# Kernel tuning notes

Measured on AMD Instinct MI355X. Metric: run time of the kernel, lower is better.

The kernel has to match this reference:

```python
import jax, jax.numpy as jnp
import numpy as np

ENCODER_DIM, DECODER_DIM, ATTENTION_DIM = 2048, 512, 512
B, L = 128, 196


def setup_inputs() -> dict:
    key = jax.random.key(0)
    ks = jax.random.split(key, 8)
    s_u = 1.0 / np.sqrt(ENCODER_DIM)
    s_w = 1.0 / np.sqrt(DECODER_DIM)
    s_a = 1.0 / np.sqrt(ATTENTION_DIM)
    return {
        "features": jax.random.normal(ks[0], (B, L, ENCODER_DIM), jnp.float32),
        "hidden_state": jax.random.normal(ks[1], (B, DECODER_DIM), jnp.float32),
        "U_w": jax.random.uniform(ks[2], (ENCODER_DIM, ATTENTION_DIM), jnp.float32, -s_u, s_u),
        "U_b": jax.random.uniform(ks[3], (ATTENTION_DIM,), jnp.float32, -s_u, s_u),
        "W_w": jax.random.uniform(ks[4], (DECODER_DIM, ATTENTION_DIM), jnp.float32, -s_w, s_w),
        "W_b": jax.random.uniform(ks[5], (ATTENTION_DIM,), jnp.float32, -s_w, s_w),
        "A_w": jax.random.uniform(ks[6], (ATTENTION_DIM,), jnp.float32, -s_a, s_a),
        "A_b": jax.random.uniform(ks[7], (1,), jnp.float32, -s_a, s_a),
    }


def reference(features, hidden_state, U_w, U_b, W_w, W_b, A_w, A_b):
    # u_hs: [B, L, A], w_ah: [B, A]
    u_hs = jnp.einsum('ble,ea->bla', features, U_w) + U_b
    w_ah = hidden_state @ W_w + W_b
    combined = jnp.tanh(u_hs + w_ah[:, None, :])          # [B, L, A]
    scores = jnp.einsum('bla,a->bl', combined, A_w) + A_b[0]  # [B, L]
    alpha = jax.nn.softmax(scores, axis=1)                 # [B, L]
    context = jnp.einsum('bl,ble->be', alpha, features)    # [B, E]
    return alpha, context
```

## Files before the change

### kernel.cpp

```cpp
#include <hip/hip_runtime.h>
#include <hip/hip_bf16.h>

#define ENC 2048
#define ADIM 512
#define DEC 512
#define NBATCH 128
#define NL 196
#define MTOT (NBATCH * NL)

typedef __attribute__((ext_vector_type(8))) short short8;
typedef __attribute__((ext_vector_type(4))) float f32x4;

__device__ __forceinline__ unsigned short f2bf(float f) {
    __hip_bfloat16 h = __float2bfloat16(f);
    union { __hip_bfloat16 h; unsigned short u; } cv; cv.h = h; return cv.u;
}
__device__ __forceinline__ unsigned int f2bf2(float lo, float hi) {
    __hip_bfloat162 h = __float22bfloat162_rn(float2{lo, hi});
    union { __hip_bfloat162 h; unsigned int u; } cv; cv.h = h; return cv.u;
}

__device__ __forceinline__ void load_lds16(const void* g, void* l) {
    __builtin_amdgcn_global_load_lds(
        (const __attribute__((address_space(1))) unsigned int*)g,
        (__attribute__((address_space(3))) unsigned int*)l, 16, 0, 0);
}

__global__ void wah_kernel(const float* __restrict__ hidden, const float* __restrict__ Ww,
                           const float* __restrict__ Wb, float* __restrict__ wah) {
    __shared__ __align__(16) float hs[DEC];
    const int b = blockIdx.x, a = threadIdx.x;
    hs[a] = hidden[b * DEC + a];
    __syncthreads();
    float acc = Wb[a];
    #pragma unroll 4
    for (int d = 0; d < DEC; d += 4) {
        f32x4 h = *(const f32x4*)&hs[d];
        acc += h.x * Ww[(d    ) * ADIM + a];
        acc += h.y * Ww[(d + 1) * ADIM + a];
        acc += h.z * Ww[(d + 2) * ADIM + a];
        acc += h.w * Ww[(d + 3) * ADIM + a];
    }
    wah[b * ADIM + a] = acc;
}

__global__ void transpose_uw(const float* __restrict__ Uw, unsigned short* __restrict__ uwT) {
    __shared__ float t[32][33];
    const int k0 = blockIdx.x * 32, n0 = blockIdx.y * 32;
    const int tx = threadIdx.x, ty = threadIdx.y;
    #pragma unroll
    for (int i = 0; i < 4; ++i)
        t[ty + 8 * i][tx] = Uw[(size_t)(k0 + ty + 8 * i) * ADIM + n0 + tx];
    __syncthreads();
    #pragma unroll
    for (int i = 0; i < 4; ++i)
        uwT[(size_t)(n0 + ty + 8 * i) * ENC + k0 + tx] = f2bf(t[tx][ty + 8 * i]);
}

__global__ __launch_bounds__(256, 3) void gemm_score_kernel(
    const float* __restrict__ feat, const unsigned short* __restrict__ uwT,
    const float* __restrict__ Ub, const float* __restrict__ wahb,
    const float* __restrict__ Aw, float* __restrict__ part)
{
    __shared__ __align__(16) unsigned char As[32768];
    __shared__ __align__(16) unsigned char Bs[16384];

    const int tid  = threadIdx.x;
    const int lane = tid & 63;
    const int w    = tid >> 6;
    const int wr   = w >> 1, wc = w & 1;
    const int l15  = lane & 15, ldr = lane >> 4;

    const int bid  = blockIdx.x;
    const int work = (bid & 7) * 98 + (bid >> 3);
    const int mb   = work >> 2;
    const int nbk  = work & 3;

    const char* featb = (const char*)feat;
    const char* uwTb  = (const char*)uwT;
    const char* aSrc[8];
    #pragma unroll
    for (int c = 0; c < 8; ++c) {
        const int row   = w * 32 + c * 4 + ldr;
        const int inner = (l15 * 16) ^ (ldr << 5) ^ ((c & 1) << 4);
        aSrc[c] = featb + (size_t)(mb * 128 + row) * (ENC * 4) + inner;
    }
    const char* bSrc[4];
    #pragma unroll
    for (int c = 0; c < 4; ++c) {
        const int n     = w * 32 + c * 8 + (lane >> 3);
        const int inner = ((lane & 7) * 16) ^ (((lane >> 3) & 7) << 4);
        bSrc[c] = uwTb + (size_t)(nbk * 128 + n) * (ENC * 2) + inner;
    }
    unsigned char* aDst = As + w * 8192;
    unsigned char* bDst = Bs + w * 4096;

    const int sA = ((l15 & 3) << 5) | ((l15 & 4) << 2);
    int abyte[4][2][2], bbyte[4][2];
    #pragma unroll
    for (int f = 0; f < 4; ++f) {
        const int r = wr * 64 + f * 16 + l15;
        const int n = wc * 64 + f * 16 + l15;
        #pragma unroll
        for (int ks = 0; ks < 2; ++ks) {
            const int k4 = ks * 128 + ldr * 32;
            abyte[f][ks][0] = r * 256 + ((k4     ) ^ sA);
            abyte[f][ks][1] = r * 256 + ((k4 + 16) ^ sA);
            bbyte[f][ks]    = n * 128 + ((ks * 64 + ldr * 16) ^ ((n & 7) << 4));
        }
    }

    f32x4 acc[4][4];
    #pragma unroll
    for (int i = 0; i < 4; ++i)
        #pragma unroll
        for (int j = 0; j < 4; ++j)
            acc[i][j] = (f32x4){0.f, 0.f, 0.f, 0.f};

    #pragma unroll 1
    for (int kt = 0; kt < 32; ++kt) {
        __syncthreads();
        #pragma unroll
        for (int c = 0; c < 8; ++c)
            load_lds16(aSrc[c] + (size_t)kt * 256, aDst + c * 1024);
        #pragma unroll
        for (int c = 0; c < 4; ++c)
            load_lds16(bSrc[c] + (size_t)kt * 128, bDst + c * 1024);
        __syncthreads();

        #pragma unroll
        for (int ks = 0; ks < 2; ++ks) {
            short8 af[4], bf[4];
            #pragma unroll
            for (int f = 0; f < 4; ++f) {
                f32x4 lo = *(const f32x4*)(As + abyte[f][ks][0]);
                f32x4 hi = *(const f32x4*)(As + abyte[f][ks][1]);
                union { unsigned int u[4]; short8 s; } cv;
                cv.u[0] = f2bf2(lo.x, lo.y);
                cv.u[1] = f2bf2(lo.z, lo.w);
                cv.u[2] = f2bf2(hi.x, hi.y);
                cv.u[3] = f2bf2(hi.z, hi.w);
                af[f] = cv.s;
                bf[f] = *(const short8*)(Bs + bbyte[f][ks]);
            }
            #pragma unroll
            for (int fm = 0; fm < 4; ++fm)
                #pragma unroll
                for (int fn = 0; fn < 4; ++fn)
                    acc[fm][fn] = __builtin_amdgcn_mfma_f32_16x16x32_bf16(
                        af[fm], bf[fn], acc[fm][fn], 0, 0, 0);
        }
    }

    float ub4[4], aw4[4]; int cidx[4];
    #pragma unroll
    for (int f = 0; f < 4; ++f) {
        const int c = nbk * 128 + wc * 64 + f * 16 + l15;
        cidx[f] = c; ub4[f] = Ub[c]; aw4[f] = Aw[c];
    }
    #pragma unroll
    for (int fm = 0; fm < 4; ++fm) {
        #pragma unroll
        for (int r = 0; r < 4; ++r) {
            const int m = mb * 128 + wr * 64 + fm * 16 + ldr * 4 + r;
            const int b = m / NL;
            const float* wrow = wahb + b * ADIM;
            float s = 0.f;
            #pragma unroll
            for (int f = 0; f < 4; ++f)
                s += aw4[f] * tanhf(acc[fm][f][r] + ub4[f] + wrow[cidx[f]]);
            s += __shfl_xor(s, 1);
            s += __shfl_xor(s, 2);
            s += __shfl_xor(s, 4);
            s += __shfl_xor(s, 8);
            if (l15 == 0) part[(nbk * 2 + wc) * MTOT + m] = s;
        }
    }
}

__global__ void softmax_kernel(const float* __restrict__ part, const float* __restrict__ Ab,
                               float* __restrict__ alpha) {
    const int b = blockIdx.x, t = threadIdx.x;
    float sv = 0.f;
    if (t < NL) {
        sv = Ab[0];
        #pragma unroll
        for (int p = 0; p < 8; ++p) sv += part[p * MTOT + b * NL + t];
    }
    float v = (t < NL) ? sv : -3.4e38f;
    #pragma unroll
    for (int o = 32; o >= 1; o >>= 1) v = fmaxf(v, __shfl_xor(v, o));
    __shared__ float rm[4], rs[4];
    if ((t & 63) == 0) rm[t >> 6] = v;
    __syncthreads();
    const float bm = fmaxf(fmaxf(rm[0], rm[1]), fmaxf(rm[2], rm[3]));
    const float e = (t < NL) ? expf(sv - bm) : 0.f;
    float s = e;
    #pragma unroll
    for (int o = 32; o >= 1; o >>= 1) s += __shfl_xor(s, o);
    if ((t & 63) == 0) rs[t >> 6] = s;
    __syncthreads();
    const float bs = rs[0] + rs[1] + rs[2] + rs[3];
    if (t < NL) alpha[b * NL + t] = e / bs;
}

__global__ void context_kernel(const float* __restrict__ feat, const float* __restrict__ alpha,
                               float* __restrict__ ctx) {
    __shared__ float al[NL];
    const int b = blockIdx.x, chunk = blockIdx.y, t = threadIdx.x;
    for (int i = t; i < NL; i += 128) al[i] = alpha[b * NL + i];
    __syncthreads();
    const int e0 = chunk * 512 + t * 4;
    const float* fp = feat + (size_t)b * NL * ENC + e0;
    f32x4 acc0 = (f32x4){0.f, 0.f, 0.f, 0.f};
    f32x4 acc1 = (f32x4){0.f, 0.f, 0.f, 0.f};
    #pragma unroll 2
    for (int l = 0; l < NL; l += 2) {
        f32x4 f0 = *(const f32x4*)(fp + (size_t)l * ENC);
        f32x4 f1 = *(const f32x4*)(fp + (size_t)(l + 1) * ENC);
        acc0 += al[l] * f0;
        acc1 += al[l + 1] * f1;
    }
    f32x4 rsum = acc0 + acc1;
    *(f32x4*)(ctx + (size_t)b * ENC + e0) = rsum;
}

extern "C" void kernel_launch(void* const* d_in, const int* in_sizes, int n_in,
                              void* d_out, int out_size, void* d_ws, size_t ws_size,
                              hipStream_t stream) {
    const float* feat   = (const float*)d_in[0];
    const float* hidden = (const float*)d_in[1];
    const float* Uw     = (const float*)d_in[2];
    const float* Ub     = (const float*)d_in[3];
    const float* Ww     = (const float*)d_in[4];
    const float* Wb     = (const float*)d_in[5];
    const float* Aw     = (const float*)d_in[6];
    const float* Ab     = (const float*)d_in[7];

    float* out   = (float*)d_out;
    float* alpha = out;
    float* ctx   = out + MTOT;

    char* ws = (char*)d_ws;
    float*          wahb = (float*)ws;
    unsigned short* uwT  = (unsigned short*)(ws + 262144);
    float*          partb= (float*)(ws + 262144 + 2097152);

    wah_kernel<<<dim3(128), dim3(512), 0, stream>>>(hidden, Ww, Wb, wahb);
    transpose_uw<<<dim3(64, 16), dim3(32, 8), 0, stream>>>(Uw, uwT);
    gemm_score_kernel<<<dim3(784), dim3(256), 0, stream>>>(feat, uwT, Ub, wahb, Aw, partb);
    softmax_kernel<<<dim3(128), dim3(256), 0, stream>>>(partb, Ab, alpha);
    context_kernel<<<dim3(128, 4), dim3(128), 0, stream>>>(feat, alpha, ctx);
}
```

Measured before the change: 186.0 us.

## Pre-pack U_w into MFMA fragment layout and double-buffer bf16 A tile in LDS

The transpose kernel now writes U_w as bf16 already arranged in MFMA fragment order, so the GEMM reads B fragments directly from global into registers with no LDS staging. The fp32 features are loaded into registers, converted to bf16 once per element, and written to a double-buffered LDS tile. Loads for the next k-step are issued while the current step's MFMAs run, with setprio raised around the compute. This removes the fp32 LDS footprint and the redundant conversions done on every LDS fragment read, and halves the barriers per k-step, at the cost of more registers and a hand-built software pipeline.

```diff
diff --git a/kernel.cpp b/kernel.cpp
--- a/kernel.cpp
+++ b/kernel.cpp
@@ -7,9 +7,11 @@
 #define NBATCH 128
 #define NL 196
 #define MTOT (NBATCH * NL)
+#define NKT 32
 
 typedef __attribute__((ext_vector_type(8))) short short8;
 typedef __attribute__((ext_vector_type(4))) float f32x4;
+typedef __attribute__((ext_vector_type(4))) unsigned int u32x4;
 
 __device__ __forceinline__ unsigned short f2bf(float f) {
     __hip_bfloat16 h = __float2bfloat16(f);
@@ -18,12 +20,6 @@
 __device__ __forceinline__ unsigned int f2bf2(float lo, float hi) {
     __hip_bfloat162 h = __float22bfloat162_rn(float2{lo, hi});
     union { __hip_bfloat162 h; unsigned int u; } cv; cv.h = h; return cv.u;
-}
-
-__device__ __forceinline__ void load_lds16(const void* g, void* l) {
-    __builtin_amdgcn_global_load_lds(
-        (const __attribute__((address_space(1))) unsigned int*)g,
-        (__attribute__((address_space(3))) unsigned int*)l, 16, 0, 0);
 }
 
 __global__ void wah_kernel(const float* __restrict__ hidden, const float* __restrict__ Ww,
@@ -44,7 +40,7 @@
     wah[b * ADIM + a] = acc;
 }
 
-__global__ void transpose_uw(const float* __restrict__ Uw, unsigned short* __restrict__ uwT) {
+__global__ void transpose_uw_frag(const float* __restrict__ Uw, unsigned short* __restrict__ uwTf) {
     __shared__ float t[32][33];
     const int k0 = blockIdx.x * 32, n0 = blockIdx.y * 32;
     const int tx = threadIdx.x, ty = threadIdx.y;
@@ -52,18 +48,25 @@
     for (int i = 0; i < 4; ++i)
         t[ty + 8 * i][tx] = Uw[(size_t)(k0 + ty + 8 * i) * ADIM + n0 + tx];
     __syncthreads();
-    #pragma unroll
-    for (int i = 0; i < 4; ++i)
-        uwT[(size_t)(n0 + ty + 8 * i) * ENC + k0 + tx] = f2bf(t[tx][ty + 8 * i]);
-}
-
-__global__ __launch_bounds__(256, 3) void gemm_score_kernel(
-    const float* __restrict__ feat, const unsigned short* __restrict__ uwT,
+    const int kf  = k0 >> 5;
+    const int nf  = (n0 >> 4) + (tx >> 4);
+    const int l15 = tx & 15;
+    const int ldr = ty >> 1, j0 = (ty & 1) * 4;
+    const int kl0 = ty * 4;
+    unsigned int lo = f2bf2(t[kl0 + 0][tx], t[kl0 + 1][tx]);
+    unsigned int hi = f2bf2(t[kl0 + 2][tx], t[kl0 + 3][tx]);
+    unsigned int* dst = (unsigned int*)(uwTf + ((size_t)((nf * 64 + kf) * 64 + ldr * 16 + l15)) * 8 + j0);
+    dst[0] = lo;
+    dst[1] = hi;
+}
+
+__global__ __launch_bounds__(256, 3) void gemm_score(
+    const float* __restrict__ feat, const unsigned short* __restrict__ uwTf,
     const float* __restrict__ Ub, const float* __restrict__ wahb,
     const float* __restrict__ Aw, float* __restrict__ part)
 {
-    __shared__ __align__(16) unsigned char As[32768];
-    __shared__ __align__(16) unsigned char Bs[16384];
+    __shared__ __align__(16) unsigned char Ab0[16384];
+    __shared__ __align__(16) unsigned char Ab1[16384];
 
     const int tid  = threadIdx.x;
     const int lane = tid & 63;
@@ -76,38 +79,22 @@
     const int mb   = work >> 2;
     const int nbk  = work & 3;
 
-    const char* featb = (const char*)feat;
-    const char* uwTb  = (const char*)uwT;
-    const char* aSrc[8];
-    #pragma unroll
-    for (int c = 0; c < 8; ++c) {
-        const int row   = w * 32 + c * 4 + ldr;
-        const int inner = (l15 * 16) ^ (ldr << 5) ^ ((c & 1) << 4);
-        aSrc[c] = featb + (size_t)(mb * 128 + row) * (ENC * 4) + inner;
-    }
-    const char* bSrc[4];
-    #pragma unroll
-    for (int c = 0; c < 4; ++c) {
-        const int n     = w * 32 + c * 8 + (lane >> 3);
-        const int inner = ((lane & 7) * 16) ^ (((lane >> 3) & 7) << 4);
-        bSrc[c] = uwTb + (size_t)(nbk * 128 + n) * (ENC * 2) + inner;
-    }
-    unsigned char* aDst = As + w * 8192;
-    unsigned char* bDst = Bs + w * 4096;
-
-    const int sA = ((l15 & 3) << 5) | ((l15 & 4) << 2);
-    int abyte[4][2][2], bbyte[4][2];
+    const int r_ = tid >> 1, h_ = tid & 1;
+    const float* aSrc = feat + (size_t)(mb * 128 + r_) * ENC + h_ * 32;
+    int wA[4];
+    #pragma unroll
+    for (int j = 0; j < 4; ++j)
+        wA[j] = r_ * 128 + (((h_ * 4 + j) ^ (r_ & 7)) << 4);
+
+    const unsigned short* bBase = uwTf + ((size_t)(nbk * 8 + wc * 4) * 4096 + (size_t)lane) * 8;
+
+    int abyte[4][2];
     #pragma unroll
     for (int f = 0; f < 4; ++f) {
-        const int r = wr * 64 + f * 16 + l15;
-        const int n = wc * 64 + f * 16 + l15;
-        #pragma unroll
-        for (int ks = 0; ks < 2; ++ks) {
-            const int k4 = ks * 128 + ldr * 32;
-            abyte[f][ks][0] = r * 256 + ((k4     ) ^ sA);
-            abyte[f][ks][1] = r * 256 + ((k4 + 16) ^ sA);
-            bbyte[f][ks]    = n * 128 + ((ks * 64 + ldr * 16) ^ ((n & 7) << 4));
-        }
+        const int ra = wr * 64 + f * 16 + l15;
+        #pragma unroll
+        for (int ks = 0; ks < 2; ++ks)
+            abyte[f][ks] = ra * 128 + (((ks * 4 + ldr) ^ (ra & 7)) << 4);
     }
 
     f32x4 acc[4][4];
@@ -117,40 +104,76 @@
         for (int j = 0; j < 4; ++j)
             acc[i][j] = (f32x4){0.f, 0.f, 0.f, 0.f};
 
+    f32x4 ar[8];
+    short8 be[8];
+
+#define ISSUE_B(KT) {                                                         \
+    _Pragma("unroll")                                                         \
+    for (int f = 0; f < 4; ++f)                                               \
+        _Pragma("unroll")                                                     \
+        for (int ks = 0; ks < 2; ++ks)                                        \
+            be[f * 2 + ks] = *(const short8*)(bBase + f * 32768 + ((KT) * 2 + ks) * 512); \
+    __builtin_amdgcn_sched_barrier(0);                                        \
+}
+#define LOAD_A(KT) {                                                          \
+    const f32x4* p = (const f32x4*)(aSrc + (size_t)(KT) * 64);                \
+    _Pragma("unroll")                                                         \
+    for (int j = 0; j < 8; ++j) ar[j] = p[j];                                 \
+    __builtin_amdgcn_sched_barrier(0);                                        \
+}
+#define CVTW(AB) {                                                            \
+    _Pragma("unroll")                                                         \
+    for (int j = 0; j < 4; ++j) {                                             \
+        u32x4 wv;                                                             \
+        wv.x = f2bf2(ar[2*j].x,   ar[2*j].y);                                 \
+        wv.y = f2bf2(ar[2*j].z,   ar[2*j].w);                                 \
+        wv.z = f2bf2(ar[2*j+1].x, ar[2*j+1].y);                               \
+        wv.w = f2bf2(ar[2*j+1].z, ar[2*j+1].w);                               \
+        *(u32x4*)((AB) + wA[j]) = wv;                                         \
+    }                                                                         \
+}
+#define COMPUTE(AB) {                                                         \
+    __builtin_amdgcn_s_setprio(1);                                            \
+    _Pragma("unroll")                                                         \
+    for (int ks = 0; ks < 2; ++ks) {                                          \
+        short8 af[4];                                                         \
+        _Pragma("unroll")                                                     \
+        for (int f = 0; f < 4; ++f)                                           \
+            af[f] = *(const short8*)((AB) + abyte[f][ks]);                    \
+        _Pragma("unroll")                                                     \
+        for (int fm = 0; fm < 4; ++fm)                                        \
+            _Pragma("unroll")                                                 \
+            for (int fn = 0; fn < 4; ++fn)                                    \
+                acc[fm][fn] = __builtin_amdgcn_mfma_f32_16x16x32_bf16(        \
+                    af[fm], be[fn * 2 + ks], acc[fm][fn], 0, 0, 0);           \
+    }                                                                         \
+    __builtin_amdgcn_s_setprio(0);                                            \
+    __builtin_amdgcn_sched_barrier(0);                                        \
+}
+
+    LOAD_A(0);
+    CVTW(Ab0);
+    __syncthreads();
+
     #pragma unroll 1
-    for (int kt = 0; kt < 32; ++kt) {
+    for (int kt = 0; kt < NKT; kt += 2) {
+        const int k1 = kt + 1;
+        const int k2 = (kt + 2 < NKT) ? kt + 2 : NKT - 1;
+        ISSUE_B(kt);
+        LOAD_A(k1);
+        COMPUTE(Ab0);
+        CVTW(Ab1);
         __syncthreads();
-        #pragma unroll
-        for (int c = 0; c < 8; ++c)
-            load_lds16(aSrc[c] + (size_t)kt * 256, aDst + c * 1024);
-        #pragma unroll
-        for (int c = 0; c < 4; ++c)
-            load_lds16(bSrc[c] + (size_t)kt * 128, bDst + c * 1024);
+        ISSUE_B(k1);
+        LOAD_A(k2);
+        COMPUTE(Ab1);
+        CVTW(Ab0);
         __syncthreads();
-
-        #pragma unroll
-        for (int ks = 0; ks < 2; ++ks) {
-            short8 af[4], bf[4];
-            #pragma unroll
-            for (int f = 0; f < 4; ++f) {
-                f32x4 lo = *(const f32x4*)(As + abyte[f][ks][0]);
-                f32x4 hi = *(const f32x4*)(As + abyte[f][ks][1]);
-                union { unsigned int u[4]; short8 s; } cv;
-                cv.u[0] = f2bf2(lo.x, lo.y);
-                cv.u[1] = f2bf2(lo.z, lo.w);
-                cv.u[2] = f2bf2(hi.x, hi.y);
-                cv.u[3] = f2bf2(hi.z, hi.w);
-                af[f] = cv.s;
-                bf[f] = *(const short8*)(Bs + bbyte[f][ks]);
-            }
-            #pragma unroll
-            for (int fm = 0; fm < 4; ++fm)
-                #pragma unroll
-                for (int fn = 0; fn < 4; ++fn)
-                    acc[fm][fn] = __builtin_amdgcn_mfma_f32_16x16x32_bf16(
-                        af[fm], bf[fn], acc[fm][fn], 0, 0, 0);
-        }
-    }
+    }
+#undef ISSUE_B
+#undef LOAD_A
+#undef CVTW
+#undef COMPUTE
 
     float ub4[4], aw4[4]; int cidx[4];
     #pragma unroll
@@ -242,13 +265,13 @@
     float* ctx   = out + MTOT;
 
     char* ws = (char*)d_ws;
-    float*          wahb = (float*)ws;
-    unsigned short* uwT  = (unsigned short*)(ws + 262144);
-    float*          partb= (float*)(ws + 262144 + 2097152);
+    float*          wahb  = (float*)ws;
+    unsigned short* uwTf  = (unsigned short*)(ws + 262144);
+    float*          partb = (float*)(ws + 262144 + 2097152);
 
     wah_kernel<<<dim3(128), dim3(512), 0, stream>>>(hidden, Ww, Wb, wahb);
-    transpose_uw<<<dim3(64, 16), dim3(32, 8), 0, stream>>>(Uw, uwT);
-    gemm_score_kernel<<<dim3(784), dim3(256), 0, stream>>>(feat, uwT, Ub, wahb, Aw, partb);
+    transpose_uw_frag<<<dim3(64, 16), dim3(32, 8), 0, stream>>>(Uw, uwTf);
+    gemm_score<<<dim3(784), dim3(256), 0, stream>>>(feat, uwTf, Ub, wahb, Aw, partb);
     softmax_kernel<<<dim3(128), dim3(256), 0, stream>>>(partb, Ab, alpha);
     context_kernel<<<dim3(128, 4), dim3(128), 0, stream>>>(feat, alpha, ctx);
 }
```

Result: slower. 233.7 us (+25.6%).
